# Kernel tuning notes

Measured on AMD Instinct MI355X. Metric: run time of the kernel, lower is better.

Reference implementation:

```python
import jax, jax.numpy as jnp
import numpy as np

TAU_MEM = 20.0
TAU_SYN = 5.0
THRESHOLD = 1.0
SURROGATE_BETA = 4.0
RESET_POTENTIAL = 0.0

B, T, D_IN, H = 32, 1024, 512, 512


def setup_inputs() -> dict:
    key = jax.random.key(0)
    k1, k2 = jax.random.split(key)
    inputs = jax.random.normal(k1, (B, T, D_IN), dtype=jnp.float32)
    kernel = jax.random.normal(k2, (D_IN, H), dtype=jnp.float32) / np.sqrt(D_IN)
    bias = jnp.zeros((H,), dtype=jnp.float32)
    return {"inputs": inputs, "kernel": kernel, "bias": bias}


def reference(inputs, kernel, bias):
    batch = inputs.shape[0]
    hidden = kernel.shape[1]
    alpha_mem = jnp.exp(jnp.float32(-1.0 / TAU_MEM))
    alpha_syn = jnp.exp(jnp.float32(-1.0 / TAU_SYN))

    # Batch the per-step dense GEMM across time: [B,T,Din] @ [Din,H] -> [B,T,H]
    currents = jnp.einsum('bti,ih->bth', inputs, kernel) + bias
    currents_t = jnp.swapaxes(currents, 0, 1)  # [T,B,H] for scan

    def step(carry, ic):
        v_mem, i_syn = carry
        i_syn = alpha_syn * i_syn + ic
        v_mem = alpha_mem * v_mem + (1.0 - alpha_mem) * i_syn
        spikes = (v_mem >= THRESHOLD).astype(jnp.float32)
        surrogate = SURROGATE_BETA / (2.0 * (1.0 + jnp.cosh(SURROGATE_BETA * (v_mem - THRESHOLD))))
        spikes_with_grad = spikes + jax.lax.stop_gradient(spikes - surrogate)
        v_mem = jnp.where(spikes > 0, RESET_POTENTIAL, v_mem)
        return (v_mem, i_syn), (spikes_with_grad, v_mem)

    init = (jnp.zeros((batch, hidden), jnp.float32), jnp.zeros((batch, hidden), jnp.float32))
    (v_final, _), (spikes_t, vmem_t) = jax.lax.scan(step, init, currents_t)

    spike_output = jnp.swapaxes(spikes_t, 0, 1)      # [B,T,H]
    membrane_states = jnp.swapaxes(vmem_t, 0, 1)     # [B,T,H]
    spike_rate = jnp.mean(spike_output)
    return spike_output, membrane_states, v_final, spike_rate
```

## Files before the change

### kernel.cpp

```cpp
#include <hip/hip_runtime.h>

typedef unsigned short ushort_t;
typedef unsigned int   uint_t;
typedef float    float4v __attribute__((ext_vector_type(4)));
typedef _Float16 h16x8   __attribute__((ext_vector_type(8)));

#define Bsz 32
#define Tsz 1024
#define Din 512
#define Hsz 512
#define Mtot (Bsz * Tsz)
#define ELEMS ((size_t)Mtot * Hsz)

#define GLL16(gp, lp) __builtin_amdgcn_global_load_lds(                        \
    (const __attribute__((address_space(1))) unsigned int*)(gp),               \
    (__attribute__((address_space(3))) unsigned int*)(lp), 16, 0, 0)

#define GLL4(gp, lp) __builtin_amdgcn_global_load_lds(                         \
    (const __attribute__((address_space(1))) unsigned int*)(gp),               \
    (__attribute__((address_space(3))) unsigned int*)(lp), 4, 0, 0)

__global__ __launch_bounds__(256) void split_fp16x2(
    const float* __restrict__ A, const float* __restrict__ W,
    _Float16* __restrict__ Ah, _Float16* __restrict__ Bh)
{
    const int bid = blockIdx.x, tid = threadIdx.x;
    if (bid < 4096) {
        const size_t e   = ((size_t)bid * 256 + tid) * 16;
        const int    row = (int)(e >> 9);
        const int    col = (int)(e & 511);
        const float4* Af = (const float4*)(A + e);
        h16x8 v0a, v1a, v0b, v1b;
#pragma unroll
        for (int q = 0; q < 4; ++q) {
            float4 x = Af[q];
            const float c[4] = {x.x, x.y, x.z, x.w};
#pragma unroll
            for (int j = 0; j < 4; ++j) {
                const float xs = c[j] * 256.0f;
                const _Float16 h0 = (_Float16)xs;
                const float rf = xs - (float)h0;
                const _Float16 h1 = (_Float16)rf;
                const int idx = q * 4 + j;
                if (idx < 8) { v0a[idx] = h0; v1a[idx] = h1; }
                else         { v0b[idx - 8] = h0; v1b[idx - 8] = h1; }
            }
        }
        _Float16* d0 = Ah + (size_t)row * 1024 + col;
        *(h16x8*)(d0)           = v0a;
        *(h16x8*)(d0 + 8)       = v0b;
        *(h16x8*)(d0 + 512)     = v1a;
        *(h16x8*)(d0 + 512 + 8) = v1b;
    } else {
        const int f4 = (bid - 4096) * 256 + tid;
        const int k  = f4 >> 7;
        const int n4 = (f4 & 127) << 2;
        float4 x = *(const float4*)(W + (size_t)k * Hsz + n4);
        const float c[4] = {x.x, x.y, x.z, x.w};
#pragma unroll
        for (int j = 0; j < 4; ++j) {
            const float ws = c[j] * 2048.0f;
            const _Float16 h0 = (_Float16)ws;
            const float rf = ws - (float)h0;
            const _Float16 h1 = (_Float16)rf;
            _Float16* d = Bh + (size_t)(n4 + j) * 1024 + k;
            d[0]   = h0;
            d[512] = h1;
        }
    }
}

#define SA_STAGE(LIMB, KK, SLOTBASE) do {                                      \
    const char* g_ = Ag + (size_t)((LIMB) * 1024) + (size_t)((KK) * 64);       \
    _Pragma("unroll") for (int H = 0; H < 4; ++H)                              \
        GLL16(g_ + (size_t)H * 131072, ldsA + (SLOTBASE) + H * 4096 + lsd);    \
} while (0)

#define SB_STAGE(LIMB, KK, SLOT) do {                                          \
    const char* g_ = Bg + (size_t)((LIMB) * 1024) + (size_t)((KK) * 64);       \
    _Pragma("unroll") for (int H = 0; H < 2; ++H)                              \
        GLL16(g_ + (size_t)H * 131072, ldsB + (SLOT) * 8192 + H * 4096 + lsd); \
} while (0)

#define LD_AF(SLOTBASE) do {                                                   \
    _Pragma("unroll") for (int mf = 0; mf < 8; ++mf)                           \
        af[mf] = *(const h16x8*)(ldsA + (SLOTBASE) + (wm + mf * 16 + lr) * 64  \
                                 + physf * 16);                                \
} while (0)

#define LD_BF(DST, SLOT) do {                                                  \
    _Pragma("unroll") for (int nf = 0; nf < 4; ++nf)                           \
        DST[nf] = *(const h16x8*)(ldsB + (SLOT) * 8192 + (wn + nf * 16 + lr)   \
                                  * 64 + physf * 16);                          \
} while (0)

#define MFMAH(BF) do { __builtin_amdgcn_s_setprio(1);                          \
    _Pragma("unroll") for (int mf = 0; mf < 8; ++mf)                           \
    _Pragma("unroll") for (int nf = 0; nf < 4; ++nf)                           \
        acc[mf][nf] = __builtin_amdgcn_mfma_f32_16x16x32_f16(                  \
            af[mf], BF[nf], acc[mf][nf], 0, 0, 0);                             \
    __builtin_amdgcn_s_setprio(0); } while (0)

#define GATE(N) do { asm volatile("s_waitcnt vmcnt(" #N ")" ::: "memory");     \
    __builtin_amdgcn_sched_barrier(0); __builtin_amdgcn_s_barrier();           \
    asm volatile("" ::: "memory"); } while (0)

__global__ __launch_bounds__(256, 2) void gemm_f16k3(
    const _Float16* __restrict__ Ah, const _Float16* __restrict__ Bh,
    const float* __restrict__ bias, float* __restrict__ C)
{
    __shared__ __align__(16) char lds[65536];
    char* ldsA = lds;
    char* ldsB = lds + 32768;

    const int tid = threadIdx.x;
    const int bid = blockIdx.x;
    const int lin = ((bid & 7) << 6) | (bid >> 3);
    const int m0  = (lin >> 2) << 8;
    const int n0  = (lin & 3) << 7;
    const int w = tid >> 6, lane = tid & 63;
    const int wm = (w & 1) << 7;
    const int wn = (w >> 1) << 6;
    const int lr = lane & 15, lg = lane >> 4;

    const int physf = lg ^ (lr & 3) ^ ((lr >> 2) & 3);

    const int srow = tid >> 2;
    const int schk = tid & 3;
    const int logchk = schk ^ (srow & 3) ^ ((srow >> 2) & 3);
    const int lsd = tid * 16;
    const char* Ag = (const char*)Ah + (size_t)(m0 + srow) * 2048 + logchk * 16;
    const char* Bg = (const char*)Bh + (size_t)(n0 + srow) * 2048 + logchk * 16;

    float4v acc[8][4];
#pragma unroll
    for (int i = 0; i < 8; ++i)
#pragma unroll
        for (int j = 0; j < 4; ++j) acc[i][j] = (float4v)0.f;

    h16x8 af[8], bf0[4], bf1[4];

    SA_STAGE(0, 0, 0);
    SB_STAGE(0, 0, 0); SB_STAGE(1, 0, 1);
    SB_STAGE(0, 1, 2); SB_STAGE(1, 1, 3);
    GATE(0);

#pragma unroll 1
    for (int k = 0; k < 15; ++k) {
        const int s0 = (2 * k) & 3, s1 = (2 * k + 1) & 3;
        GATE(4);
        LD_AF(0); LD_BF(bf0, s0);
        SA_STAGE(1, k, 16384);
        MFMAH(bf0);
        GATE(4);
        LD_BF(bf1, s1);
        SA_STAGE(0, k + 1, 0);
        MFMAH(bf1);
        GATE(4);
        LD_AF(16384);
        if (k < 14) { SB_STAGE(0, k + 2, s0); SB_STAGE(1, k + 2, s1); }
        MFMAH(bf0);
    }
    {
        GATE(0);
        LD_AF(0); LD_BF(bf0, 2);
        SA_STAGE(1, 15, 16384);
        MFMAH(bf0);
        GATE(4);
        LD_BF(bf1, 3);
        MFMAH(bf1);
        GATE(0);
        LD_AF(16384);
        MFMAH(bf0);
    }

    constexpr float INVS = 1.0f / 524288.0f;
#pragma unroll
    for (int nf = 0; nf < 4; ++nf) {
        const int col = n0 + wn + nf * 16 + lr;
        const float bv = bias[col];
#pragma unroll
        for (int mf = 0; mf < 8; ++mf)
#pragma unroll
            for (int j = 0; j < 4; ++j) {
                const int row = m0 + wm + mf * 16 + lg * 4 + j;
                C[(size_t)row * Hsz + col] = fmaf(acc[mf][nf][j], INVS, bv);
            }
    }
}

#define BM 128
#define BN 128
#define BK 16
#define LDSA (BM + 4)
#define LDSB (BN + 4)
__global__ __launch_bounds__(256) void sgemm_currents(
    const float* __restrict__ A, const float* __restrict__ B,
    const float* __restrict__ bias, float* __restrict__ C)
{
    __shared__ float As[BK][LDSA];
    __shared__ float Bs[BK][LDSB];
    const int tid = threadIdx.x;
    const int tx = tid & 15, ty = tid >> 4;
    const int m0 = blockIdx.y * BM, n0 = blockIdx.x * BN;
    const int arow = tid >> 2, ac4 = (tid & 3) * 4;
    const int brow = tid >> 5, bc4 = (tid & 31) * 4;
    float acc[8][8];
#pragma unroll
    for (int i = 0; i < 8; ++i)
#pragma unroll
        for (int j = 0; j < 8; ++j) acc[i][j] = 0.f;
    const float* Abase = A + (size_t)(m0 + arow) * Din + ac4;
    const float* Bbase = B + (size_t)brow * Hsz + n0 + bc4;
    float4 a0 = *(const float4*)Abase;
    float4 a1 = *(const float4*)(Abase + (size_t)64 * Din);
    float4 b0 = *(const float4*)Bbase;
    float4 b1 = *(const float4*)(Bbase + (size_t)8 * Hsz);
    const int NKT = Din / BK;
    for (int kt = 0; kt < NKT; ++kt) {
        const float* apf = (const float*)&a0;
        const float* aqf = (const float*)&a1;
#pragma unroll
        for (int j = 0; j < 4; ++j) As[ac4 + j][arow] = apf[j];
#pragma unroll
        for (int j = 0; j < 4; ++j) As[ac4 + j][arow + 64] = aqf[j];
        *(float4*)&Bs[brow][bc4] = b0;
        *(float4*)&Bs[brow + 8][bc4] = b1;
        __syncthreads();
        if (kt + 1 < NKT) {
            const float* An = Abase + (kt + 1) * BK;
            const float* Bn = Bbase + (size_t)(kt + 1) * BK * Hsz;
            a0 = *(const float4*)An;
            a1 = *(const float4*)(An + (size_t)64 * Din);
            b0 = *(const float4*)Bn;
            b1 = *(const float4*)(Bn + (size_t)8 * Hsz);
        }
#pragma unroll
        for (int k = 0; k < BK; ++k) {
            float4 af0 = *(const float4*)&As[k][ty * 8];
            float4 af1 = *(const float4*)&As[k][ty * 8 + 4];
            float4 bf0 = *(const float4*)&Bs[k][tx * 8];
            float4 bf1 = *(const float4*)&Bs[k][tx * 8 + 4];
            const float av[8] = {af0.x, af0.y, af0.z, af0.w, af1.x, af1.y, af1.z, af1.w};
            const float bv[8] = {bf0.x, bf0.y, bf0.z, bf0.w, bf1.x, bf1.y, bf1.z, bf1.w};
#pragma unroll
            for (int i = 0; i < 8; ++i)
#pragma unroll
                for (int j = 0; j < 8; ++j) acc[i][j] = fmaf(av[i], bv[j], acc[i][j]);
        }
        __syncthreads();
    }
    const float4 bi0 = *(const float4*)&bias[n0 + tx * 8];
    const float4 bi1 = *(const float4*)&bias[n0 + tx * 8 + 4];
#pragma unroll
    for (int i = 0; i < 8; ++i) {
        const size_t row = (size_t)(m0 + ty * 8 + i);
        float4 o0 = make_float4(acc[i][0] + bi0.x, acc[i][1] + bi0.y,
                                acc[i][2] + bi0.z, acc[i][3] + bi0.w);
        float4 o1 = make_float4(acc[i][4] + bi1.x, acc[i][5] + bi1.y,
                                acc[i][6] + bi1.z, acc[i][7] + bi1.w);
        float* cp = C + row * Hsz + n0 + tx * 8;
        *(float4*)cp = o0;
        *(float4*)(cp + 4) = o1;
    }
}

__global__ __launch_bounds__(64) void lif_scan_g(
    const float* __restrict__ cur, float* __restrict__ spikes,
    float* __restrict__ vmem, float* __restrict__ vfinal,
    float* __restrict__ partials)
{
    __shared__ __align__(16) float lbuf[2][32][64];

    constexpr float A_M  = 0.95122942450071400910f;
    constexpr float OM_M = 1.0f - A_M;
    constexpr float A_S  = 0.81873075307798182354f;

    const int tid   = threadIdx.x;
    const int bid   = blockIdx.x;
    const int batch = bid >> 3;
    const int hbase = (bid & 7) << 6;
    const size_t sbase = (size_t)batch * (size_t)(Tsz * Hsz) + hbase + tid;

    const float* gsrc = cur + sbase;
    float* gspk = spikes + sbase;
    float* gvmm = vmem + sbase;

#pragma unroll
    for (int r = 0; r < 32; ++r)
        GLL4(gsrc + r * 512, &lbuf[0][r][0]);
    asm volatile("s_waitcnt vmcnt(0)" ::: "memory");
    __builtin_amdgcn_sched_barrier(0);

    float v = 0.f, isyn = 0.f, acc = 0.f;
    int pb = 0;
#pragma unroll 1
    for (int c = 0; c < 32; ++c) {
        if (c < 31) {
            const float* gs = gsrc + (size_t)(c + 1) * 16384;
            float (*db)[64] = lbuf[pb ^ 1];
#pragma unroll
            for (int r = 0; r < 32; ++r)
                GLL4(gs + r * 512, &db[r][0]);
        }
        const float* lrow = &lbuf[pb][0][tid];
        float* sp = gspk + (size_t)c * 16384;
        float* vp = gvmm + (size_t)c * 16384;
#pragma unroll
        for (int r = 0; r < 32; ++r) {
            const float cval = lrow[r * 64];
            isyn = fmaf(A_S, isyn, cval);
            v    = fmaf(A_M, v, OM_M * isyn);
            const bool sb = (v >= 1.0f);
            float x = fmaf(4.0f, v, -4.0f);
            x = fminf(x, 30.0f);
            const float ep = __expf(x);
            const float tt = 1.0f + ep;
            const float rr = __builtin_amdgcn_rcpf(tt * tt);
            const float spk = sb ? 1.0f : 0.0f;
            const float so = fmaf(-4.0f * ep, rr, spk + spk);
            v = sb ? 0.0f : v;
            acc += so;
            sp[r * 512] = so;
            vp[r * 512] = v;
        }
        asm volatile("s_waitcnt vmcnt(0)" ::: "memory");
        __builtin_amdgcn_sched_barrier(0);
        pb ^= 1;
    }

    vfinal[bid * 64 + tid] = v;
#pragma unroll
    for (int o = 32; o; o >>= 1) acc += __shfl_down(acc, o);
    if (tid == 0) partials[blockIdx.x] = acc;
}

__device__ __forceinline__ void lif_step(float c, float& v, float& isyn,
                                         float& so_out)
{
    constexpr float A_M  = 0.95122942450071400910f;
    constexpr float OM_M = 1.0f - A_M;
    constexpr float A_S  = 0.81873075307798182354f;
    isyn = fmaf(A_S, isyn, c);
    v    = fmaf(A_M, v, OM_M * isyn);
    const float sp = (v >= 1.0f) ? 1.0f : 0.0f;
    float x = fmaf(4.0f, v, -4.0f);
    x = fminf(x, 30.0f);
    const float ep = __expf(x);
    const float tt = 1.0f + ep;
    const float surr = 4.0f * ep * __builtin_amdgcn_rcpf(tt * tt);
    so_out = fmaf(2.0f, sp, -surr);
    v = (sp > 0.f) ? 0.0f : v;
}

__global__ __launch_bounds__(64) void lif_scan(
    const float* cur, float* spikes, float* vmem, float* vfinal, float* partials)
{
    const int tid = threadIdx.x;
    const int gid = blockIdx.x * 64 + tid;
    const size_t base = ((size_t)(gid >> 9)) * (size_t)Tsz * Hsz + (gid & 511);

    float v = 0.f, isyn = 0.f, acc = 0.f;
    constexpr int P = 8;
    float ring[P];
#pragma unroll
    for (int p = 0; p < P; ++p) ring[p] = cur[base + (size_t)p * Hsz];

    for (int t = 0; t < Tsz; t += P) {
#pragma unroll
        for (int p = 0; p < P; ++p) {
            const float c = ring[p];
            int tn = t + P + p;
            tn = tn < (Tsz - 1) ? tn : (Tsz - 1);
            ring[p] = cur[base + (size_t)tn * Hsz];

            float so;
            lif_step(c, v, isyn, so);
            const size_t idx = base + (size_t)(t + p) * Hsz;
            spikes[idx] = so;
            vmem[idx]   = v;
            acc += so;
        }
    }
    vfinal[gid] = v;
#pragma unroll
    for (int off = 32; off; off >>= 1) acc += __shfl_down(acc, off);
    if (tid == 0) partials[blockIdx.x] = acc;
}

__global__ __launch_bounds__(256) void rate_finalize(
    const float* __restrict__ partials, float* __restrict__ rate)
{
    const int tid = threadIdx.x;
    float s = partials[tid];
#pragma unroll
    for (int off = 32; off; off >>= 1) s += __shfl_down(s, off);
    __shared__ float wsum[4];
    if ((tid & 63) == 0) wsum[tid >> 6] = s;
    __syncthreads();
    if (tid == 0)
        rate[0] = ((wsum[0] + wsum[1]) + (wsum[2] + wsum[3])) * (1.0f / 16777216.0f);
}

extern "C" void kernel_launch(void* const* d_in, const int* in_sizes, int n_in,
                              void* d_out, int out_size, void* d_ws, size_t ws_size,
                              hipStream_t stream)
{
    const float* inputs = (const float*)d_in[0];
    const float* weight = (const float*)d_in[1];
    const float* bias   = (const float*)d_in[2];

    float* out    = (float*)d_out;
    float* spikes = out;
    float* vmem   = out + ELEMS;
    float* vfinal = out + 2 * ELEMS;
    float* rate   = vfinal + (size_t)Bsz * Hsz;

    float* partials = (float*)d_ws;
    char*  ws       = (char*)d_ws;

    const size_t CUR_B = ELEMS * 4;
    const size_t AH_B  = (size_t)Mtot * 1024 * 2;
    const size_t BH_B  = (size_t)Hsz * 1024 * 2;

    _Float16 *Ah, *Bh;
    float* cur;
    int path;
    if (ws_size >= 4096 + CUR_B + AH_B + BH_B) {
        cur = (float*)(ws + 4096);
        Ah  = (_Float16*)(ws + 4096 + CUR_B);
        Bh  = Ah + (size_t)Mtot * 1024;
        path = 0;
    } else if (ws_size >= 4096 + CUR_B) {
        cur = (float*)(ws + 4096);
        Ah  = (_Float16*)d_out;
        Bh  = Ah + (size_t)Mtot * 1024;
        path = 1;
    } else {
        cur = vmem;
        Ah = Bh = nullptr;
        path = 2;
    }

    if (path != 2) {
        split_fp16x2<<<dim3(4096 + 256), 256, 0, stream>>>(inputs, weight, Ah, Bh);
        gemm_f16k3<<<dim3(512), 256, 0, stream>>>(Ah, Bh, bias, cur);
        lif_scan_g<<<dim3(256), 64, 0, stream>>>(cur, spikes, vmem, vfinal, partials);
    } else {
        sgemm_currents<<<dim3(4, 256), 256, 0, stream>>>(inputs, weight, bias, cur);
        lif_scan<<<dim3(256), 64, 0, stream>>>(cur, spikes, vmem, vfinal, partials);
    }
    rate_finalize<<<dim3(1), 256, 0, stream>>>(partials, rate);
}
```

Before: 153.9 us.

## Split surrogate and rate computation out of sequential LIF scan into parallel pass

After: 157.0 us. 2.0% more time.

```diff
diff --git a/kernel.cpp b/kernel.cpp
--- a/kernel.cpp
+++ b/kernel.cpp
@@ -266,9 +266,8 @@
 }
 
 __global__ __launch_bounds__(64) void lif_scan_g(
-    const float* __restrict__ cur, float* __restrict__ spikes,
-    float* __restrict__ vmem, float* __restrict__ vfinal,
-    float* __restrict__ partials)
+    const float* __restrict__ cur, float* __restrict__ vpre_out,
+    float* __restrict__ vfinal)
 {
     __shared__ __align__(16) float lbuf[2][32][64];
 
@@ -283,8 +282,7 @@
     const size_t sbase = (size_t)batch * (size_t)(Tsz * Hsz) + hbase + tid;
 
     const float* gsrc = cur + sbase;
-    float* gspk = spikes + sbase;
-    float* gvmm = vmem + sbase;
+    float* gpre = vpre_out + sbase;
 
 #pragma unroll
     for (int r = 0; r < 32; ++r)
@@ -292,7 +290,7 @@
     asm volatile("s_waitcnt vmcnt(0)" ::: "memory");
     __builtin_amdgcn_sched_barrier(0);
 
-    float v = 0.f, isyn = 0.f, acc = 0.f;
+    float v = 0.f, isyn = 0.f;
     int pb = 0;
 #pragma unroll 1
     for (int c = 0; c < 32; ++c) {
@@ -304,35 +302,74 @@
                 GLL4(gs + r * 512, &db[r][0]);
         }
         const float* lrow = &lbuf[pb][0][tid];
-        float* sp = gspk + (size_t)c * 16384;
-        float* vp = gvmm + (size_t)c * 16384;
+        float* pp = gpre + (size_t)c * 16384;
 #pragma unroll
         for (int r = 0; r < 32; ++r) {
-            const float cval = lrow[r * 64];
-            isyn = fmaf(A_S, isyn, cval);
+            isyn = fmaf(A_S, isyn, lrow[r * 64]);
             v    = fmaf(A_M, v, OM_M * isyn);
-            const bool sb = (v >= 1.0f);
-            float x = fmaf(4.0f, v, -4.0f);
-            x = fminf(x, 30.0f);
+            pp[r * 512] = v;
+            v = (v >= 1.0f) ? 0.0f : v;
+        }
+        asm volatile("s_waitcnt vmcnt(0)" ::: "memory");
+        __builtin_amdgcn_sched_barrier(0);
+        pb ^= 1;
+    }
+
+    vfinal[bid * 64 + tid] = v;
+}
+
+__global__ __launch_bounds__(256) void surr_rate(
+    float* __restrict__ spk, float* __restrict__ vmm,
+    float* __restrict__ partials)
+{
+    const int tid = threadIdx.x, bid = blockIdx.x;
+    float4* sp4 = (float4*)spk;
+    float4* vm4 = (float4*)vmm;
+    const size_t b0 = (size_t)bid * 2048 + tid;
+    float lacc = 0.f;
+#pragma unroll
+    for (int q = 0; q < 8; ++q) {
+        const size_t i = b0 + (size_t)q * 256;
+        float4 p = sp4[i];
+        const float pv[4] = {p.x, p.y, p.z, p.w};
+        float so[4], vp[4];
+#pragma unroll
+        for (int j = 0; j < 4; ++j) {
+            const bool sb = (pv[j] >= 1.0f);
+            float x = fminf(fmaf(4.0f, pv[j], -4.0f), 30.0f);
             const float ep = __expf(x);
             const float tt = 1.0f + ep;
             const float rr = __builtin_amdgcn_rcpf(tt * tt);
-            const float spk = sb ? 1.0f : 0.0f;
-            const float so = fmaf(-4.0f * ep, rr, spk + spk);
-            v = sb ? 0.0f : v;
-            acc += so;
-            sp[r * 512] = so;
-            vp[r * 512] = v;
-        }
-        asm volatile("s_waitcnt vmcnt(0)" ::: "memory");
-        __builtin_amdgcn_sched_barrier(0);
-        pb ^= 1;
-    }
-
-    vfinal[bid * 64 + tid] = v;
-#pragma unroll
-    for (int o = 32; o; o >>= 1) acc += __shfl_down(acc, o);
-    if (tid == 0) partials[blockIdx.x] = acc;
+            const float s2 = sb ? 2.0f : 0.0f;
+            so[j] = fmaf(-4.0f * ep, rr, s2);
+            vp[j] = sb ? 0.0f : pv[j];
+            lacc += so[j];
+        }
+        sp4[i] = make_float4(so[0], so[1], so[2], so[3]);
+        vm4[i] = make_float4(vp[0], vp[1], vp[2], vp[3]);
+    }
+#pragma unroll
+    for (int o = 32; o; o >>= 1) lacc += __shfl_down(lacc, o);
+    __shared__ float wsum[4];
+    if ((tid & 63) == 0) wsum[tid >> 6] = lacc;
+    __syncthreads();
+    if (tid == 0) partials[bid] = (wsum[0] + wsum[1]) + (wsum[2] + wsum[3]);
+}
+
+__global__ __launch_bounds__(256) void rate_finalize2(
+    const float* __restrict__ partials, float* __restrict__ rate)
+{
+    const int tid = threadIdx.x;
+    float s = 0.f;
+#pragma unroll
+    for (int q = 0; q < 8; ++q) s += partials[q * 256 + tid];
+#pragma unroll
+    for (int o = 32; o; o >>= 1) s += __shfl_down(s, o);
+    __shared__ float wsum[4];
+    if ((tid & 63) == 0) wsum[tid >> 6] = s;
+    __syncthreads();
+    if (tid == 0)
+        rate[0] = ((wsum[0] + wsum[1]) + (wsum[2] + wsum[3])) * (1.0f / 16777216.0f);
 }
 
 __device__ __forceinline__ void lif_step(float c, float& v, float& isyn,
@@ -419,6 +456,7 @@
     float* partials = (float*)d_ws;
     char*  ws       = (char*)d_ws;
 
+    const size_t HDR   = 16384;
     const size_t CUR_B = ELEMS * 4;
     const size_t AH_B  = (size_t)Mtot * 1024 * 2;
     const size_t BH_B  = (size_t)Hsz * 1024 * 2;
@@ -426,13 +464,13 @@
     _Float16 *Ah, *Bh;
     float* cur;
     int path;
-    if (ws_size >= 4096 + CUR_B + AH_B + BH_B) {
-        cur = (float*)(ws + 4096);
-        Ah  = (_Float16*)(ws + 4096 + CUR_B);
+    if (ws_size >= HDR + CUR_B + AH_B + BH_B) {
+        cur = (float*)(ws + HDR);
+        Ah  = (_Float16*)(ws + HDR + CUR_B);
         Bh  = Ah + (size_t)Mtot * 1024;
         path = 0;
-    } else if (ws_size >= 4096 + CUR_B) {
-        cur = (float*)(ws + 4096);
+    } else if (ws_size >= HDR + CUR_B) {
+        cur = (float*)(ws + HDR);
         Ah  = (_Float16*)d_out;
         Bh  = Ah + (size_t)Mtot * 1024;
         path = 1;
@@ -445,10 +483,12 @@
     if (path != 2) {
         split_fp16x2<<<dim3(4096 + 256), 256, 0, stream>>>(inputs, weight, Ah, Bh);
         gemm_f16k3<<<dim3(512), 256, 0, stream>>>(Ah, Bh, bias, cur);
-        lif_scan_g<<<dim3(256), 64, 0, stream>>>(cur, spikes, vmem, vfinal, partials);
+        lif_scan_g<<<dim3(256), 64, 0, stream>>>(cur, spikes, vfinal);
+        surr_rate<<<dim3(2048), 256, 0, stream>>>(spikes, vmem, partials);
+        rate_finalize2<<<dim3(1), 256, 0, stream>>>(partials, rate);
     } else {
         sgemm_currents<<<dim3(4, 256), 256, 0, stream>>>(inputs, weight, bias, cur);
         lif_scan<<<dim3(256), 64, 0, stream>>>(cur, spikes, vmem, vfinal, partials);
-    }
-    rate_finalize<<<dim3(1), 256, 0, stream>>>(partials, rate);
-}
+        rate_finalize<<<dim3(1), 256, 0, stream>>>(partials, rate);
+    }
+}
```
